# Optimization experiments

Measured on AMD Instinct MI355X. Metric: run time of the kernel, lower is better.

## Reference

```python
import jax, jax.numpy as jnp
import numpy as np

HIDDEN = 1024
NUM_HEADS = 16
HEAD_DIM = HIDDEN // NUM_HEADS


def setup_inputs() -> dict:
    key = jax.random.key(0)
    k1, k2, k3 = jax.random.split(key, 3)
    x = jax.random.normal(k1, (2, 2048, HIDDEN), dtype=jnp.float32)
    # Linear weights, torch layout [out_features, in_features]
    w_qkv = jax.random.normal(k2, (3 * HIDDEN, HIDDEN), dtype=jnp.float32) * 0.02
    w_out = jax.random.normal(k3, (HIDDEN, HIDDEN), dtype=jnp.float32) * 0.02
    return {"x": x, "w_qkv": w_qkv, "w_out": w_out}


def reference(x, w_qkv, w_out):
    B, S, H = x.shape
    scale = 1.0 / HEAD_DIM ** 0.5
    qkv = jnp.einsum('bsh,oh->bso', x, w_qkv)              # [B,S,3H]
    qkv = qkv.reshape(B, S, 3, NUM_HEADS, HEAD_DIM)
    qkv = jnp.transpose(qkv, (2, 0, 3, 1, 4))               # [3,B,nh,S,hd]
    q, k, v = qkv[0], qkv[1], qkv[2]
    scores = jnp.einsum('bnsd,bntd->bnst', q, k) * scale    # [B,nh,S,S]
    attn = jax.nn.softmax(scores, axis=-1)
    out = jnp.einsum('bnst,bntd->bnsd', attn, v)            # [B,nh,S,hd]
    out = jnp.transpose(out, (0, 2, 1, 3)).reshape(B, S, H)
    return jnp.einsum('bsh,oh->bso', out, w_out)
```

## Files before the change

### kernel.cpp

```cpp
#include <hip/hip_runtime.h>
#include <stdint.h>

typedef unsigned short u16;
typedef __bf16 bf16x8 __attribute__((ext_vector_type(8)));
typedef float f32x4 __attribute__((ext_vector_type(4)));
typedef float f32x16 __attribute__((ext_vector_type(16)));
typedef unsigned u32x4 __attribute__((ext_vector_type(4)));

#define DEVI __device__ __forceinline__

typedef __attribute__((address_space(1))) void gvoid;
typedef __attribute__((address_space(3))) void lvoid;

DEVI u16 f2b(float f) {
  unsigned x = __builtin_bit_cast(unsigned, f);
  return (u16)((x + 0x7fffu + ((x >> 16) & 1u)) >> 16);
}

DEVI float exp2g(float x) { return __builtin_amdgcn_exp2f(x); }

DEVI void gload_lds16(const void* g, void* l) {
  __builtin_amdgcn_global_load_lds((gvoid*)g, (lvoid*)l, 16, 0, 0);
}

#define QSCALE 0.18033688011112042f

__global__ void cast_x(const float* __restrict__ in, u16* __restrict__ out, int n4) {
  int i = blockIdx.x * 256 + threadIdx.x;
  int stride = gridDim.x * 256;
  for (; i < n4; i += stride) {
    float4 v = ((const float4*)in)[i];
    ushort4 o;
    o.x = f2b(v.x); o.y = f2b(v.y); o.z = f2b(v.z); o.w = f2b(v.w);
    ((ushort4*)out)[i] = o;
  }
}

__global__ void cast_w(const float* __restrict__ wqkv, const float* __restrict__ wout,
                       u16* __restrict__ outb) {
  int i = blockIdx.x * 256 + threadIdx.x;
  int stride = gridDim.x * 256;
  for (; i < 1048576; i += stride) {
    const float* src = (i < 786432) ? wqkv + 4 * (long)i : wout + 4 * (long)(i - 786432);
    float4 v = *(const float4*)src;
    if (i < 262144) { v.x *= QSCALE; v.y *= QSCALE; v.z *= QSCALE; v.w *= QSCALE; }
    ushort4 o;
    o.x = f2b(v.x); o.y = f2b(v.y); o.z = f2b(v.z); o.w = f2b(v.w);
    ((ushort4*)outb)[i] = o;
  }
}

template<bool BF16OUT>
__global__ __launch_bounds__(256)
void gemm_bt(const u16* __restrict__ A, const u16* __restrict__ B, void* __restrict__ Cv,
             int M, int N, int K) {
  __shared__ u16 lA[128 * 64];
  __shared__ u16 lB[128 * 64];
  const int tid = threadIdx.x;
  const int lane = tid & 63;
  const int lr = lane & 15;
  const int lg = lane >> 4;
  const int wid = tid >> 6;
  const long bm = (long)blockIdx.y * 128;
  const long bn = (long)blockIdx.x * 128;
  const int wr = (wid >> 1) * 64;
  const int wc = (wid & 1) * 64;

  f32x4 acc[4][4];
#pragma unroll
  for (int i = 0; i < 4; ++i)
#pragma unroll
    for (int j = 0; j < 4; ++j)
      acc[i][j] = (f32x4){0.f, 0.f, 0.f, 0.f};

  for (int k0 = 0; k0 < K; k0 += 64) {
#pragma unroll
    for (int q = 0; q < 4; ++q) {
      int bi = tid + q * 256;
      int row = bi >> 3;
      int col = ((bi & 7) ^ (row & 7)) * 8;
      gload_lds16(A + (bm + row) * (long)K + k0 + col, (char*)lA + bi * 16);
    }
#pragma unroll
    for (int q = 0; q < 4; ++q) {
      int bi = tid + q * 256;
      int row = bi >> 3;
      int col = ((bi & 7) ^ (row & 7)) * 8;
      gload_lds16(B + (bn + row) * (long)K + k0 + col, (char*)lB + bi * 16);
    }
    __syncthreads();
#pragma unroll
    for (int kk = 0; kk < 2; ++kk) {
      bf16x8 af[4], bfr[4];
      int kb = kk * 4 + lg;
#pragma unroll
      for (int mi = 0; mi < 4; ++mi) {
        int row = wr + mi * 16 + lr;
        af[mi] = *(const bf16x8*)((const char*)lA + row * 128 + ((kb ^ (row & 7)) << 4));
      }
#pragma unroll
      for (int ni = 0; ni < 4; ++ni) {
        int row = wc + ni * 16 + lr;
        bfr[ni] = *(const bf16x8*)((const char*)lB + row * 128 + ((kb ^ (row & 7)) << 4));
      }
#pragma unroll
      for (int mi = 0; mi < 4; ++mi)
#pragma unroll
        for (int ni = 0; ni < 4; ++ni)
          acc[mi][ni] = __builtin_amdgcn_mfma_f32_16x16x32_bf16(af[mi], bfr[ni], acc[mi][ni], 0, 0, 0);
    }
    __syncthreads();
  }
#pragma unroll
  for (int mi = 0; mi < 4; ++mi)
#pragma unroll
    for (int ni = 0; ni < 4; ++ni)
#pragma unroll
      for (int r = 0; r < 4; ++r) {
        long row = bm + wr + mi * 16 + lg * 4 + r;
        long col = bn + wc + ni * 16 + lr;
        float v = acc[mi][ni][r];
        if (BF16OUT) ((u16*)Cv)[row * (long)N + col] = f2b(v);
        else         ((float*)Cv)[row * (long)N + col] = v;
      }
}

__global__ __launch_bounds__(256)
void transpose_v(const u16* __restrict__ qkv, u16* __restrict__ vT) {
  __shared__ u16 T[64][72];
  const int tid = threadIdx.x;
  const int t0 = blockIdx.x * 64;
  const int h  = blockIdx.y;
  const int b  = blockIdx.z;
  const int r  = tid >> 2;
  const int c0 = (tid & 3) * 16;

  const u16* src = qkv + ((long)b * 2048 + t0 + r) * 3072 + 2048 + h * 64 + c0;
  uint4 a0 = *(const uint4*)src;
  uint4 a1 = *(const uint4*)(src + 8);
  *(uint4*)&T[r][c0] = a0;
  *(uint4*)&T[r][c0 + 8] = a1;
  __syncthreads();

  u16 buf[16];
#pragma unroll
  for (int j = 0; j < 16; ++j) buf[j] = T[c0 + j][r];
  u16* dst = vT + ((long)b * 16 + h) * 131072 + r * 2048 + t0 + c0;
  *(uint4*)dst = *(const uint4*)&buf[0];
  *(uint4*)(dst + 8) = *(const uint4*)&buf[8];
}

__global__ __launch_bounds__(512, 4)
void attn_fwd(const u16* __restrict__ qkv, const u16* __restrict__ vT,
              u16* __restrict__ outb) {
  __shared__ char SM[65536];

  const int tid = threadIdx.x;
  const int lane = tid & 63;
  const int wid = tid >> 6;
  const int ql = lane & 31;
  const int h  = lane >> 5;
  const int th = wid >> 2;
  const int qb = wid & 3;
  const int qt = blockIdx.x;
  const int hd = blockIdx.y;
  const int b  = blockIdx.z;

  const long rowbase = (long)b * 2048;
  const int qcol = hd * 64;
  const int kcol = 1024 + hd * 64;
  const int TSK = 64 * 3072;
  const long vhb = ((long)b * 16 + hd) * 131072;

  const int q0w = qt * 128 + qb * 32;
  bf16x8 qf[4];
  {
    const u16* qp = qkv + (rowbase + q0w + ql) * 3072 + qcol + h * 8;
#pragma unroll
    for (int dblk = 0; dblk < 4; ++dblk)
      qf[dblk] = *(const bf16x8*)(qp + dblk * 16);
  }

  float l_r = 0.f;
  f32x16 o[2];
#pragma unroll
  for (int d = 0; d < 2; ++d)
#pragma unroll
    for (int r = 0; r < 16; ++r) o[d][r] = 0.f;

  const int rk = tid >> 3;
  const int ck = ((tid & 7) ^ (rk & 7)) * 8;
  const int dstb = tid * 16;
  const u16* kp = qkv + (rowbase + rk) * 3072 + kcol + ck;
  const u16* vp = vT + vhb + rk * 2048 + ck;

  gload_lds16(kp, SM + dstb);                 gload_lds16(vp, SM + 32768 + dstb);
  gload_lds16(kp + TSK, SM + 8192 + dstb);    gload_lds16(vp + 64, SM + 40960 + dstb);
  kp += 2 * TSK; vp += 128;
  asm volatile("s_waitcnt vmcnt(2)" ::: "memory");
  __builtin_amdgcn_s_barrier();
  __builtin_amdgcn_sched_barrier(0);

  for (int tt = 0; tt < 8; ++tt) {
#pragma unroll
    for (int I = 0; I < 4; ++I) {
      char* KsCur = SM + I * 8192;
      char* KsNxt = SM + ((I + 2) & 3) * 8192;
      char* VsCur = SM + 32768 + I * 8192;
      char* VsNxt = SM + 32768 + ((I + 2) & 3) * 8192;

      gload_lds16(kp, KsNxt + dstb);  kp += TSK;
      gload_lds16(vp, VsNxt + dstb);  vp += 64;

      f32x16 s;
#pragma unroll
      for (int r = 0; r < 16; ++r) s[r] = 0.f;
      const char* Kb = KsCur + (th * 32 + ql) * 128;
      __builtin_amdgcn_s_setprio(1);
#pragma unroll
      for (int kd = 0; kd < 4; ++kd) {
        bf16x8 kf = *(const bf16x8*)(Kb + (((kd * 2 + h) ^ (ql & 7)) << 4));
        s = __builtin_amdgcn_mfma_f32_32x32x16_bf16(kf, qf[kd], s, 0, 0, 0);
      }
      __builtin_amdgcn_s_setprio(0);

#pragma unroll
      for (int r = 0; r < 16; ++r) s[r] = exp2g(s[r]);
      l_r += (((s[0] + s[1]) + (s[2] + s[3])) + ((s[4] + s[5]) + (s[6] + s[7])))
           + (((s[8] + s[9]) + (s[10] + s[11])) + ((s[12] + s[13]) + (s[14] + s[15])));

      unsigned w[8];
#pragma unroll
      for (int m = 0; m < 8; ++m)
        asm("v_cvt_pk_bf16_f32 %0, %1, %2" : "=v"(w[m]) : "v"(s[2 * m]), "v"(s[2 * m + 1]));

      bf16x8 pb[2];
#pragma unroll
      for (int ks = 0; ks < 2; ++ks) {
        unsigned a0 = w[4 * ks],     a2 = w[4 * ks + 2];
        unsigned a1 = w[4 * ks + 1], a3 = w[4 * ks + 3];
        asm("s_nop 1\n\tv_permlane32_swap_b32 %0, %1" : "+v"(a0), "+v"(a2));
        asm("s_nop 1\n\tv_permlane32_swap_b32 %0, %1" : "+v"(a1), "+v"(a3));
        u32x4 t; t[0] = a0; t[1] = a1; t[2] = a2; t[3] = a3;
        pb[ks] = __builtin_bit_cast(bf16x8, t);
      }

      __builtin_amdgcn_s_setprio(1);
#pragma unroll
      for (int dblk = 0; dblk < 2; ++dblk) {
        const char* Vb = VsCur + (dblk * 32 + ql) * 128;
#pragma unroll
        for (int ks = 0; ks < 2; ++ks) {
          bf16x8 vf = *(const bf16x8*)(Vb + (((th * 4 + ks * 2 + h) ^ (ql & 7)) << 4));
          o[dblk] = __builtin_amdgcn_mfma_f32_32x32x16_bf16(vf, pb[ks], o[dblk], 0, 0, 0);
        }
      }
      __builtin_amdgcn_s_setprio(0);

      asm volatile("s_waitcnt vmcnt(2)" ::: "memory");
      __builtin_amdgcn_s_barrier();
      __builtin_amdgcn_sched_barrier(0);
    }
  }

  asm volatile("s_waitcnt vmcnt(0)" ::: "memory");
  __syncthreads();

  float px = l_r, py = l_r;
  asm("s_nop 1\n\tv_permlane32_swap_b32 %0, %1" : "+v"(px), "+v"(py));
  float lw = l_r + (h ? px : py);

  if (th == 1) {
    char* reg = SM + qb * 8320;
#pragma unroll
    for (int dblk = 0; dblk < 2; ++dblk)
#pragma unroll
      for (int r = 0; r < 16; ++r) {
        int dl = dblk * 32 + (r & 3) + 8 * (r >> 2) + 4 * h;
        *(float*)(reg + dl * 128 + ql * 4) = o[dblk][r];
      }
    if (h == 0) *(float*)(reg + 8192 + ql * 4) = lw;
  }
  __syncthreads();
  if (th == 0) {
    const char* reg = SM + qb * 8320;
#pragma unroll
    for (int dblk = 0; dblk < 2; ++dblk)
#pragma unroll
      for (int r = 0; r < 16; ++r) {
        int dl = dblk * 32 + (r & 3) + 8 * (r >> 2) + 4 * h;
        o[dblk][r] += *(const float*)(reg + dl * 128 + ql * 4);
      }
    float inv = 1.0f / (lw + *(const float*)(reg + 8192 + ql * 4));
    long row = rowbase + q0w + ql;
#pragma unroll
    for (int dblk = 0; dblk < 2; ++dblk)
#pragma unroll
      for (int m = 0; m < 4; ++m) {
        ushort4 st;
        st.x = f2b(o[dblk][4 * m + 0] * inv);
        st.y = f2b(o[dblk][4 * m + 1] * inv);
        st.z = f2b(o[dblk][4 * m + 2] * inv);
        st.w = f2b(o[dblk][4 * m + 3] * inv);
        *(ushort4*)(outb + row * 1024 + qcol + dblk * 32 + 8 * m + 4 * h) = st;
      }
  }
}

extern "C" void kernel_launch(void* const* d_in, const int* in_sizes, int n_in,
                              void* d_out, int out_size, void* d_ws, size_t ws_size,
                              hipStream_t stream) {
  const float* x     = (const float*)d_in[0];
  const float* w_qkv = (const float*)d_in[1];
  const float* w_out = (const float*)d_in[2];
  float* out = (float*)d_out;

  char* ws = (char*)d_ws;
  u16* xb    = (u16*)(ws);
  u16* vT    = (u16*)(ws);
  u16* wqkvb = (u16*)(ws + 8388608);
  u16* woutb = (u16*)(ws + 14680064);
  u16* qkv   = (u16*)(ws + 16777216);
  u16* attn  = (u16*)(ws + 41943040);

  cast_x<<<1024, 256, 0, stream>>>(x, xb, 4096 * 1024 / 4);
  cast_w<<<1024, 256, 0, stream>>>(w_qkv, w_out, wqkvb);

  gemm_bt<true ><<<dim3(24, 32), 256, 0, stream>>>(xb, wqkvb, qkv, 4096, 3072, 1024);
  transpose_v<<<dim3(32, 16, 2), 256, 0, stream>>>(qkv, vT);
  attn_fwd<<<dim3(16, 16, 2), 512, 0, stream>>>(qkv, vT, attn);
  gemm_bt<false><<<dim3(8, 32), 256, 0, stream>>>(attn, woutb, out, 4096, 1024, 1024);
}
```

Measured before the change: 118.6 us.

## Merge cast kernels and compute V transposed directly via swapped GEMM

Merges the two fp32-to-bf16 cast kernels into one launch. Splits the QKV projection into a Q/K GEMM and a separate V GEMM with swapped operands, so V^T is written directly in the head-major transposed layout. This removes the standalone transpose kernel and its extra round trip through memory. The cost is scattered 2-byte stores in the V GEMM epilogue and an extra GEMM launch with a smaller grid.

After: 123.1 us. +3.8%, slower.

```diff
diff --git a/kernel.cpp b/kernel.cpp
--- a/kernel.cpp
+++ b/kernel.cpp
@@ -25,32 +25,30 @@
 
 #define QSCALE 0.18033688011112042f
 
-__global__ void cast_x(const float* __restrict__ in, u16* __restrict__ out, int n4) {
+__global__ void cast_all(const float* __restrict__ x, const float* __restrict__ wqkv,
+                         const float* __restrict__ wout, u16* __restrict__ outb) {
   int i = blockIdx.x * 256 + threadIdx.x;
   int stride = gridDim.x * 256;
-  for (; i < n4; i += stride) {
-    float4 v = ((const float4*)in)[i];
+  for (; i < 2097152; i += stride) {
+    const float* src;
+    float sc = 1.0f;
+    if (i < 1048576) {
+      src = x + 4 * (long)i;
+    } else if (i < 1835008) {
+      int j = i - 1048576;
+      src = wqkv + 4 * (long)j;
+      if (j < 262144) sc = QSCALE;
+    } else {
+      src = wout + 4 * (long)(i - 1835008);
+    }
+    float4 v = *(const float4*)src;
     ushort4 o;
-    o.x = f2b(v.x); o.y = f2b(v.y); o.z = f2b(v.z); o.w = f2b(v.w);
-    ((ushort4*)out)[i] = o;
-  }
-}
-
-__global__ void cast_w(const float* __restrict__ wqkv, const float* __restrict__ wout,
-                       u16* __restrict__ outb) {
-  int i = blockIdx.x * 256 + threadIdx.x;
-  int stride = gridDim.x * 256;
-  for (; i < 1048576; i += stride) {
-    const float* src = (i < 786432) ? wqkv + 4 * (long)i : wout + 4 * (long)(i - 786432);
-    float4 v = *(const float4*)src;
-    if (i < 262144) { v.x *= QSCALE; v.y *= QSCALE; v.z *= QSCALE; v.w *= QSCALE; }
-    ushort4 o;
-    o.x = f2b(v.x); o.y = f2b(v.y); o.z = f2b(v.z); o.w = f2b(v.w);
+    o.x = f2b(v.x * sc); o.y = f2b(v.y * sc); o.z = f2b(v.z * sc); o.w = f2b(v.w * sc);
     ((ushort4*)outb)[i] = o;
   }
 }
 
-template<bool BF16OUT>
+template<int OUT>
 __global__ __launch_bounds__(256)
 void gemm_bt(const u16* __restrict__ A, const u16* __restrict__ B, void* __restrict__ Cv,
              int M, int N, int K) {
@@ -120,38 +118,17 @@
         long row = bm + wr + mi * 16 + lg * 4 + r;
         long col = bn + wc + ni * 16 + lr;
         float v = acc[mi][ni][r];
-        if (BF16OUT) ((u16*)Cv)[row * (long)N + col] = f2b(v);
-        else         ((float*)Cv)[row * (long)N + col] = v;
-      }
-}
-
-__global__ __launch_bounds__(256)
-void transpose_v(const u16* __restrict__ qkv, u16* __restrict__ vT) {
-  __shared__ u16 T[64][72];
-  const int tid = threadIdx.x;
-  const int t0 = blockIdx.x * 64;
-  const int h  = blockIdx.y;
-  const int b  = blockIdx.z;
-  const int r  = tid >> 2;
-  const int c0 = (tid & 3) * 16;
-
-  const u16* src = qkv + ((long)b * 2048 + t0 + r) * 3072 + 2048 + h * 64 + c0;
-  uint4 a0 = *(const uint4*)src;
-  uint4 a1 = *(const uint4*)(src + 8);
-  *(uint4*)&T[r][c0] = a0;
-  *(uint4*)&T[r][c0 + 8] = a1;
-  __syncthreads();
-
-  u16 buf[16];
-#pragma unroll
-  for (int j = 0; j < 16; ++j) buf[j] = T[c0 + j][r];
-  u16* dst = vT + ((long)b * 16 + h) * 131072 + r * 2048 + t0 + c0;
-  *(uint4*)dst = *(const uint4*)&buf[0];
-  *(uint4*)(dst + 8) = *(const uint4*)&buf[8];
+        if (OUT == 0)      ((u16*)Cv)[row * (long)N + col] = f2b(v);
+        else if (OUT == 1) ((float*)Cv)[row * (long)N + col] = v;
+        else {
+          long f = row, tok = col;
+          ((u16*)Cv)[(((tok >> 11) << 4) + (f >> 6)) * 131072 + (f & 63) * 2048 + (tok & 2047)] = f2b(v);
+        }
+      }
 }
 
 __global__ __launch_bounds__(512, 4)
-void attn_fwd(const u16* __restrict__ qkv, const u16* __restrict__ vT,
+void attn_fwd(const u16* __restrict__ qk, const u16* __restrict__ vT,
               u16* __restrict__ outb) {
   __shared__ char SM[65536];
 
@@ -169,13 +146,13 @@
   const long rowbase = (long)b * 2048;
   const int qcol = hd * 64;
   const int kcol = 1024 + hd * 64;
-  const int TSK = 64 * 3072;
+  const int TSK = 64 * 2048;
   const long vhb = ((long)b * 16 + hd) * 131072;
 
   const int q0w = qt * 128 + qb * 32;
   bf16x8 qf[4];
   {
-    const u16* qp = qkv + (rowbase + q0w + ql) * 3072 + qcol + h * 8;
+    const u16* qp = qk + (rowbase + q0w + ql) * 2048 + qcol + h * 8;
 #pragma unroll
     for (int dblk = 0; dblk < 4; ++dblk)
       qf[dblk] = *(const bf16x8*)(qp + dblk * 16);
@@ -191,7 +168,7 @@
   const int rk = tid >> 3;
   const int ck = ((tid & 7) ^ (rk & 7)) * 8;
   const int dstb = tid * 16;
-  const u16* kp = qkv + (rowbase + rk) * 3072 + kcol + ck;
+  const u16* kp = qk + (rowbase + rk) * 2048 + kcol + ck;
   const u16* vp = vT + vhb + rk * 2048 + ck;
 
   gload_lds16(kp, SM + dstb);                 gload_lds16(vp, SM + 32768 + dstb);
@@ -317,17 +294,18 @@
 
   char* ws = (char*)d_ws;
   u16* xb    = (u16*)(ws);
-  u16* vT    = (u16*)(ws);
   u16* wqkvb = (u16*)(ws + 8388608);
   u16* woutb = (u16*)(ws + 14680064);
-  u16* qkv   = (u16*)(ws + 16777216);
+  u16* qk    = (u16*)(ws + 16777216);
+  u16* vT    = (u16*)(ws + 33554432);
   u16* attn  = (u16*)(ws + 41943040);
 
-  cast_x<<<1024, 256, 0, stream>>>(x, xb, 4096 * 1024 / 4);
-  cast_w<<<1024, 256, 0, stream>>>(w_qkv, w_out, wqkvb);
-
-  gemm_bt<true ><<<dim3(24, 32), 256, 0, stream>>>(xb, wqkvb, qkv, 4096, 3072, 1024);
-  transpose_v<<<dim3(32, 16, 2), 256, 0, stream>>>(qkv, vT);
-  attn_fwd<<<dim3(16, 16, 2), 512, 0, stream>>>(qkv, vT, attn);
-  gemm_bt<false><<<dim3(8, 32), 256, 0, stream>>>(attn, woutb, out, 4096, 1024, 1024);
-}
+  cast_all<<<2048, 256, 0, stream>>>(x, w_qkv, w_out, xb);
+
+  gemm_bt<0><<<dim3(16, 32), 256, 0, stream>>>(xb, wqkvb, qk, 4096, 2048, 1024);
+  gemm_bt<2><<<dim3(32, 8), 256, 0, stream>>>(wqkvb + 2048 * 1024, xb, vT, 1024, 4096, 1024);
+
+  attn_fwd<<<dim3(16, 16, 2), 512, 0, stream>>>(qk, vT, attn);
+
+  gemm_bt<1><<<dim3(8, 32), 256, 0, stream>>>(attn, woutb, out, 4096, 1024, 1024);
+}
```
